# Kernel optimization log

Hardware: AMD Instinct MI355X
Metric: run time of the kernel (lower is better)

## Reference

```python
import jax, jax.numpy as jnp
import numpy as np
from jax import lax

N, XD, L, D, R = 32768, 8, 16, 64, 64
HID_E, HID_N, MIX = 256, 512, 32
LOG2PI = float(np.log(2.0 * np.pi))


def setup_inputs() -> dict:
    key = jax.random.key(0)
    ks = jax.random.split(key, 18)
    g = lambda k, shape, s: (jax.random.normal(k, shape, jnp.float32) * s)
    init_std = 0.001
    return {
        "X": jax.random.normal(ks[0], (N, XD, L), jnp.float32),
        "init_w": g(ks[1], (1, R), init_std),
        "cores": g(ks[2], (L, R, D, R), init_std),          # core_list stacked
        "enc1_w": g(ks[3], (HID_E, XD), 1.0 / np.sqrt(XD)),
        "enc1_b": jnp.zeros((HID_E,), jnp.float32),
        "enc2_w": g(ks[4], (D, HID_E), 1.0 / np.sqrt(HID_E)),
        "enc2_b": jnp.zeros((D,), jnp.float32),
        "nade_w1": g(ks[5], (HID_N, R), 1.0 / np.sqrt(R)),
        "nade_b1": jnp.zeros((HID_N,), jnp.float32),
        "nade_w2": g(ks[6], (R, HID_N), 1.0 / np.sqrt(HID_N)),
        "nade_b2": jnp.zeros((R,), jnp.float32),
        "mu_w": g(ks[7], (MIX * XD, R), 1.0 / np.sqrt(R)),
        "mu_b": jnp.zeros((MIX * XD,), jnp.float32),
        "sig_w": g(ks[8], (MIX * XD, R), 1.0 / np.sqrt(R)),
        "sig_b": jnp.zeros((MIX * XD,), jnp.float32),
        "alpha_w": g(ks[9], (MIX, R), 1.0 / np.sqrt(R)),
        "alpha_b": jnp.zeros((MIX,), jnp.float32),
    }


def _encode(x, enc1_w, enc1_b, enc2_w, enc2_b):
    # x: [..., xd] -> [..., d]  (NADE-style input encoder)
    h = jax.nn.relu(x @ enc1_w.T + enc1_b)
    return h @ enc2_w.T + enc2_b


def _phi(x, h, nade_w1, nade_b1, nade_w2, nade_b2,
         mu_w, mu_b, sig_w, sig_b, alpha_w, alpha_b):
    # x: [n, xd], h: [n, r] hidden state -> [n] mixture-of-Gaussians log-density
    n = x.shape[0]
    h = jax.nn.relu(h @ nade_w1.T + nade_b1)
    h = jax.nn.relu(h @ nade_w2.T + nade_b2)
    mu = (h @ mu_w.T + mu_b).reshape(n, MIX, XD)
    log_sig = (h @ sig_w.T + sig_b).reshape(n, MIX, XD)
    sig = jnp.exp(log_sig)
    log_alpha = jax.nn.log_softmax(h @ alpha_w.T + alpha_b, axis=-1)  # [n, MIX]
    z = (x[:, None, :] - mu) / sig
    comp_lp = jnp.sum(-0.5 * z * z - log_sig - 0.5 * LOG2PI, axis=-1)  # [n, MIX]
    return jax.nn.logsumexp(log_alpha + comp_lp, axis=-1)


def reference(X, init_w, cores, enc1_w, enc1_b, enc2_w, enc2_b,
              nade_w1, nade_b1, nade_w2, nade_b2,
              mu_w, mu_b, sig_w, sig_b, alpha_w, alpha_b):
    n = X.shape[0]
    xseq = jnp.transpose(X, (2, 0, 1))                      # [L, n, xd]
    enc_all = _encode(xseq, enc1_w, enc1_b, enc2_w, enc2_b)  # [L, n, d]
    phi = lambda x, h: _phi(x, h, nade_w1, nade_b1, nade_w2, nade_b2,
                            mu_w, mu_b, sig_w, sig_b, alpha_w, alpha_b)

    tmp0 = jnp.broadcast_to(init_w, (n, R))
    res0 = phi(xseq[0], tmp0)
    norm0 = jnp.sum(tmp0 * tmp0)

    def step(tmp, inp):
        enc_prev, core_prev, x_cur = inp
        tmp = jnp.einsum('nd,ni,idj->nj', enc_prev, tmp, core_prev)
        return tmp, (phi(x_cur, tmp), jnp.sum(tmp * tmp))

    xs = (enc_all[:L - 1], cores[:L - 1], xseq[1:])
    _, (res_steps, norm_steps) = lax.scan(step, tmp0, xs)
    result = res0 + jnp.sum(res_steps, axis=0)   # [n] log-likelihood
    norm = norm0 + jnp.sum(norm_steps)           # scalar Frobenius norm accumulator
    return result, norm
```

## Files before the change

### kernel.cpp

```cpp
#include <hip/hip_runtime.h>

typedef unsigned short u16;
typedef unsigned int u32;
typedef __attribute__((ext_vector_type(8))) __bf16 bf16x8;
typedef __attribute__((ext_vector_type(4))) float f32x4;

#define NSAMP 32768
#define HALF_LOG2PI 0.91893853320467274f

#define O_W1N 0
#define O_W2N 32768
#define O_MUW 65536
#define O_SGW 81920
#define O_ALW 98304
#define O_E1W 100352
#define O_E2W 108544
#define O_CORT 124928
#define CORT_STEP 262144
#define WS_U16 4057088

#define LH1A 0
#define LH1B 8192
#define LCLP 0
#define LALP 8192
#define LH2  16384
#define LXP  24576
#define LENC 32768
#define LTMPA 49152
#define LTMPB 57344
#define LXT  65536
#define XTS 66
#define LDS_BYTES 67648

static __device__ __forceinline__ u16 f2b(float x){ return __builtin_bit_cast(u16,(__bf16)x); }
static __device__ __forceinline__ float b2f(u16 u){ return __builtin_bit_cast(float,((u32)u)<<16); }
static __device__ __forceinline__ u32 pk2(float lo, float hi){
  return (u32)__builtin_bit_cast(u16,(__bf16)lo) | ((u32)__builtin_bit_cast(u16,(__bf16)hi)<<16);
}
static __device__ __forceinline__ f32x4 MF(uint4 a, uint4 b, f32x4 c){
  union U{uint4 q; bf16x8 v;};
  U A, B; A.q=a; B.q=b;
  return __builtin_amdgcn_mfma_f32_16x16x32_bf16(A.v, B.v, c, 0, 0, 0);
}

__global__ void prep_w(const float* __restrict__ nw1, const float* __restrict__ nw2,
                       const float* __restrict__ muw, const float* __restrict__ sgw,
                       const float* __restrict__ alw, const float* __restrict__ e1w,
                       const float* __restrict__ e2w, u16* __restrict__ ws,
                       float* __restrict__ out) {
  int idx0 = blockIdx.x * blockDim.x + threadIdx.x;
  int stride = gridDim.x * blockDim.x;
  for (int idx = idx0; idx < 124928; idx += stride) {
    float v;
    if      (idx < 32768)  v = nw1[idx];
    else if (idx < 65536)  v = nw2[idx - 32768];
    else if (idx < 81920)  v = muw[idx - 65536];
    else if (idx < 98304)  v = sgw[idx - 81920];
    else if (idx < 100352) v = alw[idx - 98304];
    else if (idx < 108544) { int j = idx - 100352; int o = j >> 5, k = j & 31;
                             v = (k < 8) ? e1w[o*8 + k] : 0.0f; }
    else                   v = e2w[idx - 108544];
    ws[idx] = f2b(v);
  }
  if (idx0 == 0) out[NSAMP] = 0.0f;
}

__global__ void prep_core(const float* __restrict__ cores, u16* __restrict__ ws) {
  int t = blockIdx.x >> 6, i = blockIdx.x & 63;
  __shared__ float T[64][65];
  const float* src = cores + ((size_t)(t*64 + i)*64)*64;
  for (int idx = threadIdx.x; idx < 4096; idx += 256) {
    int d = idx >> 6, j = idx & 63;
    T[d][j] = src[d*64 + j];
  }
  __syncthreads();
  u16* dst = ws + O_CORT + (size_t)t*CORT_STEP + (size_t)i*64;
  for (int idx = threadIdx.x; idx < 4096; idx += 256) {
    int j = idx >> 6, d = idx & 63;
    dst[(size_t)j*4096 + d] = f2b(T[d][j]);
  }
}

__global__ __launch_bounds__(256, 2)
void fused(const float* __restrict__ X, const float* __restrict__ init_w,
           const float* __restrict__ b1e, const float* __restrict__ b2e,
           const float* __restrict__ b1n, const float* __restrict__ b2n,
           const float* __restrict__ mub, const float* __restrict__ sgb,
           const float* __restrict__ alb, const u16* __restrict__ ws,
           float* __restrict__ out) {
  __shared__ __align__(16) char Lp[LDS_BYTES];
  const int tid = threadIdx.x;
  const int w = tid >> 6, l = tid & 63, li = l & 15, g = l >> 4;
  const int n0 = blockIdx.x * 64;
  const int sw = (li & 7) << 4;
  float res = 0.f, nrm = 0.f;

  char* TMPc = Lp + LTMPA;
  char* TMPn = Lp + LTMPB;

  for (int idx = tid; idx < 4096; idx += 256) {
    int s = idx >> 6, r = idx & 63;
    *(u16*)(TMPc + s*128 + ((2*r) ^ ((s & 7) << 4))) = f2b(init_w[r]);
  }
  { uint4 z = {0,0,0,0};
    for (int idx = tid; idx < 512; idx += 256) *(uint4*)(Lp + LXP + idx*16) = z; }
  if (tid < 64) { float v = init_w[tid]; nrm += 64.f * v * v; }
  __syncthreads();

  for (int t = 0; t < 16; ++t) {
    for (int idx = tid; idx < 512; idx += 256) {
      int s = idx & 63, d = idx >> 6;
      float x = X[(size_t)(n0 + s)*128 + d*16 + t];
      *(float*)(Lp + LXT + (d*XTS + s)*4) = x;
      *(u16*)(Lp + LXP + s*128 + ((2*d) ^ ((s & 7) << 4))) = f2b(x);
    }
    __syncthreads();

    f32x4 acc2[4];
#pragma unroll
    for (int st = 0; st < 4; ++st) acc2[st] = (f32x4){0.f,0.f,0.f,0.f};
#pragma unroll 1
    for (int oc = 0; oc < 8; ++oc) {
      const u16* a0 = ws + O_W1N + (oc*64 + w*16 + li)*64 + 8*g;
      uint4 af0 = *(const uint4*)a0;
      uint4 af1 = *(const uint4*)(a0 + 32);
      char* H1b = Lp + ((oc & 1) ? LH1B : LH1A);
      float4 bb = *(const float4*)(b1n + oc*64 + w*16 + 4*g);
#pragma unroll
      for (int st = 0; st < 4; ++st) {
        int s = st*16 + li;
        uint4 b0 = *(const uint4*)(TMPc + s*128 + ((16*g) ^ sw));
        uint4 b1 = *(const uint4*)(TMPc + s*128 + ((64 + 16*g) ^ sw));
        f32x4 a1 = (f32x4){0.f,0.f,0.f,0.f};
        a1 = MF(af0, b0, a1); a1 = MF(af1, b1, a1);
        float v0 = fmaxf(a1[0] + bb.x, 0.f), v1 = fmaxf(a1[1] + bb.y, 0.f);
        float v2 = fmaxf(a1[2] + bb.z, 0.f), v3 = fmaxf(a1[3] + bb.w, 0.f);
        *(u32*)(H1b + s*128 + ((32*w + 8*g) ^ sw))     = pk2(v0, v1);
        *(u32*)(H1b + s*128 + ((32*w + 8*g + 4) ^ sw)) = pk2(v2, v3);
      }
      __syncthreads();
      const u16* a2 = ws + O_W2N + (w*16 + li)*512 + oc*64 + 8*g;
      uint4 c0 = *(const uint4*)a2;
      uint4 c1 = *(const uint4*)(a2 + 32);
#pragma unroll
      for (int st = 0; st < 4; ++st) {
        int s = st*16 + li;
        uint4 b0 = *(const uint4*)(H1b + s*128 + ((16*g) ^ sw));
        uint4 b1 = *(const uint4*)(H1b + s*128 + ((64 + 16*g) ^ sw));
        acc2[st] = MF(c0, b0, acc2[st]); acc2[st] = MF(c1, b1, acc2[st]);
      }
    }
    {
      float4 bb = *(const float4*)(b2n + w*16 + 4*g);
#pragma unroll
      for (int st = 0; st < 4; ++st) {
        int s = st*16 + li;
        float v0 = fmaxf(acc2[st][0] + bb.x, 0.f), v1 = fmaxf(acc2[st][1] + bb.y, 0.f);
        float v2 = fmaxf(acc2[st][2] + bb.z, 0.f), v3 = fmaxf(acc2[st][3] + bb.w, 0.f);
        *(u32*)(Lp + LH2 + s*128 + ((32*w + 8*g) ^ sw))     = pk2(v0, v1);
        *(u32*)(Lp + LH2 + s*128 + ((32*w + 8*g + 4) ^ sw)) = pk2(v2, v3);
      }
    }
    __syncthreads();

#pragma unroll 1
    for (int c = 0; c < 4; ++c) {
      int ob = c*64 + w*16;
      const u16* as_ = ws + O_SGW + (ob + li)*64 + 8*g;
      const u16* am_ = ws + O_MUW + (ob + li)*64 + 8*g;
      uint4 sf0 = *(const uint4*)as_, sf1 = *(const uint4*)(as_ + 32);
      uint4 mf0 = *(const uint4*)am_, mf1 = *(const uint4*)(am_ + 32);
      float4 bs = *(const float4*)(sgb + ob + 4*g);
      float4 bm = *(const float4*)(mub + ob + 4*g);
      const float bsv[4] = {bs.x, bs.y, bs.z, bs.w};
      const float bmv[4] = {bm.x, bm.y, bm.z, bm.w};
#pragma unroll
      for (int st = 0; st < 4; ++st) {
        int s = st*16 + li;
        uint4 b0 = *(const uint4*)(Lp + LH2 + s*128 + ((16*g) ^ sw));
        uint4 b1 = *(const uint4*)(Lp + LH2 + s*128 + ((64 + 16*g) ^ sw));
        f32x4 aS = (f32x4){0.f,0.f,0.f,0.f}, aM = (f32x4){0.f,0.f,0.f,0.f};
        aS = MF(sf0, b0, aS); aS = MF(sf1, b1, aS);
        aM = MF(mf0, b0, aM); aM = MF(mf1, b1, aM);
        float part = 0.f;
#pragma unroll
        for (int r = 0; r < 4; ++r) {
          int d = (4*g + r) & 7;
          float ls = aS[r] + bsv[r];
          float mu = aM[r] + bmv[r];
          float xv = *(const float*)(Lp + LXT + (d*XTS + s)*4);
          float z = (xv - mu) * __expf(-ls);
          part += -0.5f*z*z - ls - HALF_LOG2PI;
        }
        float comb = part + __shfl_xor(part, 16);
        if (!(g & 1)) {
          int mix = c*8 + 2*w + (g >> 1);
          *(float*)(Lp + LCLP + (mix*64 + s)*4) = comb;
        }
      }
    }
    {
      int s = w*16 + li;
#pragma unroll
      for (int ot = 0; ot < 2; ++ot) {
        const u16* aa = ws + O_ALW + (ot*16 + li)*64 + 8*g;
        uint4 a0 = *(const uint4*)aa, a1 = *(const uint4*)(aa + 32);
        uint4 b0 = *(const uint4*)(Lp + LH2 + s*128 + ((16*g) ^ sw));
        uint4 b1 = *(const uint4*)(Lp + LH2 + s*128 + ((64 + 16*g) ^ sw));
        f32x4 acc = (f32x4){0.f,0.f,0.f,0.f};
        acc = MF(a0, b0, acc); acc = MF(a1, b1, acc);
        float4 ab4 = *(const float4*)(alb + ot*16 + 4*g);
        const float abv[4] = {ab4.x, ab4.y, ab4.z, ab4.w};
#pragma unroll
        for (int r = 0; r < 4; ++r)
          *(float*)(Lp + LALP + ((ot*16 + 4*g + r)*64 + s)*4) = acc[r] + abv[r];
      }
    }
    __syncthreads();

    if (tid < 64) {
      float m1 = -1e30f, m2 = -1e30f;
#pragma unroll 1
      for (int m = 0; m < 32; ++m) {
        float a  = *(const float*)(Lp + LALP + (m*64 + tid)*4);
        float cc = *(const float*)(Lp + LCLP + (m*64 + tid)*4);
        m1 = fmaxf(m1, a + cc); m2 = fmaxf(m2, a);
      }
      float s1 = 0.f, s2 = 0.f;
#pragma unroll 1
      for (int m = 0; m < 32; ++m) {
        float a  = *(const float*)(Lp + LALP + (m*64 + tid)*4);
        float cc = *(const float*)(Lp + LCLP + (m*64 + tid)*4);
        s1 += __expf(a + cc - m1); s2 += __expf(a - m2);
      }
      res += (m1 + __logf(s1)) - (m2 + __logf(s2));
    }
    if (t == 15) break;
    __syncthreads();

    f32x4 acE[4];
#pragma unroll
    for (int st = 0; st < 4; ++st) acE[st] = (f32x4){0.f,0.f,0.f,0.f};
#pragma unroll 1
    for (int ec = 0; ec < 4; ++ec) {
      const u16* ae_ = ws + O_E1W + (ec*64 + w*16 + li)*32 + 8*g;
      uint4 ae = *(const uint4*)ae_;
      char* H1b = Lp + ((ec & 1) ? LH1B : LH1A);
      float4 bb = *(const float4*)(b1e + ec*64 + w*16 + 4*g);
#pragma unroll
      for (int st = 0; st < 4; ++st) {
        int s = st*16 + li;
        uint4 b0 = *(const uint4*)(Lp + LXP + s*128 + ((16*g) ^ sw));
        f32x4 ah = (f32x4){0.f,0.f,0.f,0.f};
        ah = MF(ae, b0, ah);
        float v0 = fmaxf(ah[0] + bb.x, 0.f), v1 = fmaxf(ah[1] + bb.y, 0.f);
        float v2 = fmaxf(ah[2] + bb.z, 0.f), v3 = fmaxf(ah[3] + bb.w, 0.f);
        *(u32*)(H1b + s*128 + ((32*w + 8*g) ^ sw))     = pk2(v0, v1);
        *(u32*)(H1b + s*128 + ((32*w + 8*g + 4) ^ sw)) = pk2(v2, v3);
      }
      __syncthreads();
      const u16* a2 = ws + O_E2W + (w*16 + li)*256 + ec*64 + 8*g;
      uint4 c0 = *(const uint4*)a2, c1 = *(const uint4*)(a2 + 32);
#pragma unroll
      for (int st = 0; st < 4; ++st) {
        int s = st*16 + li;
        uint4 b0 = *(const uint4*)(H1b + s*128 + ((16*g) ^ sw));
        uint4 b1 = *(const uint4*)(H1b + s*128 + ((64 + 16*g) ^ sw));
        acE[st] = MF(c0, b0, acE[st]); acE[st] = MF(c1, b1, acE[st]);
      }
    }
    {
      float4 be = *(const float4*)(b2e + w*16 + 4*g);
      const float bev[4] = {be.x, be.y, be.z, be.w};
#pragma unroll
      for (int st = 0; st < 4; ++st) {
        int s = st*16 + li;
#pragma unroll
        for (int r = 0; r < 4; ++r)
          *(float*)(Lp + LENC + s*256 + ((64*w + 16*g + 4*r) ^ sw)) = acE[st][r] + bev[r];
      }
    }
    __syncthreads();

    f32x4 aU[4];
#pragma unroll
    for (int st = 0; st < 4; ++st) aU[st] = (f32x4){0.f,0.f,0.f,0.f};
    const u16* cort = ws + O_CORT + (size_t)t*CORT_STEP + (w*16 + li)*4096;
    const int bs_ = tid >> 2, bq = tid & 3;
    const int bsw = (bs_ & 7) << 4;
    auto BUILD = [&](int c) {
      int i  = 2*c + (bq >> 1);
      int d0 = (bq & 1) * 32;
      float ts = b2f(*(const u16*)(TMPc + bs_*128 + ((2*i) ^ bsw)));
      char* dst = Lp + ((c & 1) ? 16384 : 0) + bs_*256;
      const char* ef = Lp + LENC + bs_*256;
#pragma unroll
      for (int jj = 0; jj < 4; ++jj) {
        float4 e0 = *(const float4*)(ef + ((4*(d0 + 8*jj))     ^ bsw));
        float4 e1 = *(const float4*)(ef + ((4*(d0 + 8*jj + 4)) ^ bsw));
        uint4 o;
        o.x = pk2(ts*e0.x, ts*e0.y);
        o.y = pk2(ts*e0.z, ts*e0.w);
        o.z = pk2(ts*e1.x, ts*e1.y);
        o.w = pk2(ts*e1.z, ts*e1.w);
        *(uint4*)(dst + ((64*bq + 16*jj) ^ bsw)) = o;
      }
    };
    BUILD(0);
    __syncthreads();
    uint4 a0 = *(const uint4*)(cort + 8*g);
    uint4 a1 = *(const uint4*)(cort + 32 + 8*g);
    uint4 a2 = *(const uint4*)(cort + 64 + 8*g);
    uint4 a3 = *(const uint4*)(cort + 96 + 8*g);
#pragma unroll 1
    for (int c = 0; c < 32; ++c) {
      uint4 na0 = a0, na1 = a1, na2 = a2, na3 = a3;
      if (c < 31) {
        const u16* cn = cort + (c + 1)*128;
        na0 = *(const uint4*)(cn + 8*g);
        na1 = *(const uint4*)(cn + 32 + 8*g);
        na2 = *(const uint4*)(cn + 64 + 8*g);
        na3 = *(const uint4*)(cn + 96 + 8*g);
        BUILD(c + 1);
      }
      const char* Bb = Lp + ((c & 1) ? 16384 : 0);
#pragma unroll
      for (int st = 0; st < 4; ++st) {
        int s = st*16 + li;
        const char* bp = Bb + s*256;
        aU[st] = MF(a0, *(const uint4*)(bp + ((16*g) ^ sw)), aU[st]);
        aU[st] = MF(a1, *(const uint4*)(bp + ((64  + 16*g) ^ sw)), aU[st]);
        aU[st] = MF(a2, *(const uint4*)(bp + ((128 + 16*g) ^ sw)), aU[st]);
        aU[st] = MF(a3, *(const uint4*)(bp + ((192 + 16*g) ^ sw)), aU[st]);
      }
      __syncthreads();
      a0 = na0; a1 = na1; a2 = na2; a3 = na3;
    }
#pragma unroll
    for (int st = 0; st < 4; ++st) {
      int s = st*16 + li;
      nrm += aU[st][0]*aU[st][0] + aU[st][1]*aU[st][1]
           + aU[st][2]*aU[st][2] + aU[st][3]*aU[st][3];
      *(u32*)(TMPn + s*128 + ((32*w + 8*g) ^ sw))     = pk2(aU[st][0], aU[st][1]);
      *(u32*)(TMPn + s*128 + ((32*w + 8*g + 4) ^ sw)) = pk2(aU[st][2], aU[st][3]);
    }
    { uint4 z = {0,0,0,0};
      for (int idx = tid; idx < 512; idx += 256) *(uint4*)(Lp + LXP + idx*16) = z; }
    __syncthreads();
    { char* tt = TMPc; TMPc = TMPn; TMPn = tt; }
  }

  if (tid < 64) out[n0 + tid] = res;
  __syncthreads();
  *(float*)(Lp + LCLP + tid*4) = nrm;
  __syncthreads();
  if (tid < 64) {
    float v = *(const float*)(Lp + LCLP + tid*4)
            + *(const float*)(Lp + LCLP + (tid + 64)*4)
            + *(const float*)(Lp + LCLP + (tid + 128)*4)
            + *(const float*)(Lp + LCLP + (tid + 192)*4);
#pragma unroll
    for (int off = 32; off > 0; off >>= 1) v += __shfl_down(v, off);
    if (tid == 0) atomicAdd(out + NSAMP, v);
  }
}

extern "C" void kernel_launch(void* const* d_in, const int* in_sizes, int n_in,
                              void* d_out, int out_size, void* d_ws, size_t ws_size,
                              hipStream_t stream) {
  const float* X      = (const float*)d_in[0];
  const float* init_w = (const float*)d_in[1];
  const float* cores  = (const float*)d_in[2];
  const float* e1w    = (const float*)d_in[3];
  const float* b1e    = (const float*)d_in[4];
  const float* e2w    = (const float*)d_in[5];
  const float* b2e    = (const float*)d_in[6];
  const float* nw1    = (const float*)d_in[7];
  const float* b1n    = (const float*)d_in[8];
  const float* nw2    = (const float*)d_in[9];
  const float* b2n    = (const float*)d_in[10];
  const float* muw    = (const float*)d_in[11];
  const float* mub    = (const float*)d_in[12];
  const float* sgw    = (const float*)d_in[13];
  const float* sgb    = (const float*)d_in[14];
  const float* alw    = (const float*)d_in[15];
  const float* alb    = (const float*)d_in[16];
  float* out = (float*)d_out;
  u16*   ws  = (u16*)d_ws;

  prep_w<<<64, 256, 0, stream>>>(nw1, nw2, muw, sgw, alw, e1w, e2w, ws, out);
  prep_core<<<960, 256, 0, stream>>>(cores, ws);
  fused<<<NSAMP/64, 256, 0, stream>>>(X, init_w, b1e, b2e, b1n, b2n,
                                      mub, sgb, alb, ws, out);
}
```

Before: 971.5 us.

## Split-K core contraction across waves, software-pipeline MLP stages, parallelize logsumexp

The TT core contraction now splits the K dimension (i*64+d) across the four waves, with each wave computing all 64 outputs. B fragments are built in registers instead of being staged through double-buffered LDS with a barrier per chunk. Partial sums are reduced through LDS in bf16, and the core weights are pre-permuted into an MFMA-fragment layout. The two-layer NADE and encoder MLPs are software-pipelined so layer 1 of chunk p overlaps layer 2 of chunk p-1 with a single barrier per step, and the mixture logsumexp is spread over all four waves instead of one. The main intent is to remove per-chunk barriers and the serial single-wave reduction. In exchange it uses more LDS (80KB), more accumulator registers, and bf16 rounding of the partial sums.

```diff
diff --git a/kernel.cpp b/kernel.cpp
--- a/kernel.cpp
+++ b/kernel.cpp
@@ -17,23 +17,30 @@
 #define O_E2W 108544
 #define O_CORT 124928
 #define CORT_STEP 262144
-#define WS_U16 4057088
-
-#define LH1A 0
-#define LH1B 8192
-#define LCLP 0
-#define LALP 8192
-#define LH2  16384
-#define LXP  24576
-#define LENC 32768
-#define LTMPA 49152
-#define LTMPB 57344
-#define LXT  65536
-#define XTS 66
-#define LDS_BYTES 67648
+
+#define L_H1A 0
+#define L_H1B 8192
+#define L_LM1 0
+#define L_LM2 1024
+#define L_LS1 8192
+#define L_LS2 9216
+#define L_PRA 0
+#define L_PRB 8192
+#define L_PRC 16384
+#define L_H2  16384
+#define L_CLP 24576
+#define L_ALP 32768
+#define L_XT  40960
+#define L_XP  43008
+#define L_TMPA 49152
+#define L_TMPB 57344
+#define L_ENC 65536
+#define LDS_BYTES 81920
 
 static __device__ __forceinline__ u16 f2b(float x){ return __builtin_bit_cast(u16,(__bf16)x); }
 static __device__ __forceinline__ float b2f(u16 u){ return __builtin_bit_cast(float,((u32)u)<<16); }
+static __device__ __forceinline__ float b2flo(u32 v){ return __builtin_bit_cast(float, v<<16); }
+static __device__ __forceinline__ float b2fhi(u32 v){ return __builtin_bit_cast(float, v & 0xffff0000u); }
 static __device__ __forceinline__ u32 pk2(float lo, float hi){
   return (u32)__builtin_bit_cast(u16,(__bf16)lo) | ((u32)__builtin_bit_cast(u16,(__bf16)hi)<<16);
 }
@@ -67,17 +74,15 @@
 
 __global__ void prep_core(const float* __restrict__ cores, u16* __restrict__ ws) {
   int t = blockIdx.x >> 6, i = blockIdx.x & 63;
-  __shared__ float T[64][65];
-  const float* src = cores + ((size_t)(t*64 + i)*64)*64;
+  const float* src = cores + ((size_t)(t*64 + i) * 64) * 64;
+  u16* dst = ws + O_CORT + (size_t)t * CORT_STEP;
   for (int idx = threadIdx.x; idx < 4096; idx += 256) {
     int d = idx >> 6, j = idx & 63;
-    T[d][j] = src[d*64 + j];
-  }
-  __syncthreads();
-  u16* dst = ws + O_CORT + (size_t)t*CORT_STEP + (size_t)i*64;
-  for (int idx = threadIdx.x; idx < 4096; idx += 256) {
-    int j = idx >> 6, d = idx & 63;
-    dst[(size_t)j*4096 + d] = f2b(T[d][j]);
+    float v = src[d*64 + j];
+    int k = i*64 + d;
+    int kk = k >> 5, g = (k >> 3) & 3, b = k & 7;
+    int ot = j >> 4, li = j & 15;
+    dst[(size_t)(((kk*4 + ot)*64) + g*16 + li)*8 + b] = f2b(v);
   }
 }
 
@@ -91,64 +96,70 @@
   __shared__ __align__(16) char Lp[LDS_BYTES];
   const int tid = threadIdx.x;
   const int w = tid >> 6, l = tid & 63, li = l & 15, g = l >> 4;
+  const int e3 = li & 7;
+  const int sw = e3 << 4;
   const int n0 = blockIdx.x * 64;
-  const int sw = (li & 7) << 4;
   float res = 0.f, nrm = 0.f;
 
-  char* TMPc = Lp + LTMPA;
-  char* TMPn = Lp + LTMPB;
+  char* TMPc = Lp + L_TMPA;
+  char* TMPn = Lp + L_TMPB;
 
   for (int idx = tid; idx < 4096; idx += 256) {
     int s = idx >> 6, r = idx & 63;
     *(u16*)(TMPc + s*128 + ((2*r) ^ ((s & 7) << 4))) = f2b(init_w[r]);
   }
   { uint4 z = {0,0,0,0};
-    for (int idx = tid; idx < 512; idx += 256) *(uint4*)(Lp + LXP + idx*16) = z; }
+    *(uint4*)(Lp + L_XP + tid*16) = z; }
   if (tid < 64) { float v = init_w[tid]; nrm += 64.f * v * v; }
   __syncthreads();
 
   for (int t = 0; t < 16; ++t) {
     for (int idx = tid; idx < 512; idx += 256) {
-      int s = idx & 63, d = idx >> 6;
+      int d = idx >> 6, s = idx & 63;
       float x = X[(size_t)(n0 + s)*128 + d*16 + t];
-      *(float*)(Lp + LXT + (d*XTS + s)*4) = x;
-      *(u16*)(Lp + LXP + s*128 + ((2*d) ^ ((s & 7) << 4))) = f2b(x);
-    }
-    __syncthreads();
+      *(float*)(Lp + L_XT + (d*64 + s)*4) = x;
+      *(u16*)(Lp + L_XP + s*64 + ((2*d) ^ ((s & 3) << 4))) = f2b(x);
+    }
 
     f32x4 acc2[4];
 #pragma unroll
     for (int st = 0; st < 4; ++st) acc2[st] = (f32x4){0.f,0.f,0.f,0.f};
 #pragma unroll 1
-    for (int oc = 0; oc < 8; ++oc) {
-      const u16* a0 = ws + O_W1N + (oc*64 + w*16 + li)*64 + 8*g;
-      uint4 af0 = *(const uint4*)a0;
-      uint4 af1 = *(const uint4*)(a0 + 32);
-      char* H1b = Lp + ((oc & 1) ? LH1B : LH1A);
-      float4 bb = *(const float4*)(b1n + oc*64 + w*16 + 4*g);
-#pragma unroll
-      for (int st = 0; st < 4; ++st) {
-        int s = st*16 + li;
-        uint4 b0 = *(const uint4*)(TMPc + s*128 + ((16*g) ^ sw));
-        uint4 b1 = *(const uint4*)(TMPc + s*128 + ((64 + 16*g) ^ sw));
-        f32x4 a1 = (f32x4){0.f,0.f,0.f,0.f};
-        a1 = MF(af0, b0, a1); a1 = MF(af1, b1, a1);
-        float v0 = fmaxf(a1[0] + bb.x, 0.f), v1 = fmaxf(a1[1] + bb.y, 0.f);
-        float v2 = fmaxf(a1[2] + bb.z, 0.f), v3 = fmaxf(a1[3] + bb.w, 0.f);
-        *(u32*)(H1b + s*128 + ((32*w + 8*g) ^ sw))     = pk2(v0, v1);
-        *(u32*)(H1b + s*128 + ((32*w + 8*g + 4) ^ sw)) = pk2(v2, v3);
+    for (int p = 0; p <= 8; ++p) {
+      if (p < 8) {
+        const u16* a0p = ws + O_W1N + (p*64 + w*16 + li)*64 + 8*g;
+        uint4 af0 = *(const uint4*)a0p;
+        uint4 af1 = *(const uint4*)(a0p + 32);
+        float4 bb = *(const float4*)(b1n + p*64 + w*16 + 4*g);
+        char* H1b = Lp + ((p & 1) ? L_H1B : L_H1A);
+#pragma unroll
+        for (int st = 0; st < 4; ++st) {
+          int s = st*16 + li;
+          uint4 b0 = *(const uint4*)(TMPc + s*128 + ((16*g) ^ sw));
+          uint4 b1 = *(const uint4*)(TMPc + s*128 + ((64 + 16*g) ^ sw));
+          f32x4 a1 = (f32x4){0.f,0.f,0.f,0.f};
+          a1 = MF(af0, b0, a1); a1 = MF(af1, b1, a1);
+          float v0 = fmaxf(a1[0] + bb.x, 0.f), v1 = fmaxf(a1[1] + bb.y, 0.f);
+          float v2 = fmaxf(a1[2] + bb.z, 0.f), v3 = fmaxf(a1[3] + bb.w, 0.f);
+          *(u32*)(H1b + s*128 + ((32*w + 8*g) ^ sw))     = pk2(v0, v1);
+          *(u32*)(H1b + s*128 + ((32*w + 8*g + 4) ^ sw)) = pk2(v2, v3);
+        }
+      }
+      if (p > 0) {
+        int q = p - 1;
+        const u16* a2p = ws + O_W2N + (w*16 + li)*512 + q*64 + 8*g;
+        uint4 c0 = *(const uint4*)a2p;
+        uint4 c1 = *(const uint4*)(a2p + 32);
+        const char* H1r = Lp + ((q & 1) ? L_H1B : L_H1A);
+#pragma unroll
+        for (int st = 0; st < 4; ++st) {
+          int s = st*16 + li;
+          uint4 b0 = *(const uint4*)(H1r + s*128 + ((16*g) ^ sw));
+          uint4 b1 = *(const uint4*)(H1r + s*128 + ((64 + 16*g) ^ sw));
+          acc2[st] = MF(c0, b0, acc2[st]); acc2[st] = MF(c1, b1, acc2[st]);
+        }
       }
       __syncthreads();
-      const u16* a2 = ws + O_W2N + (w*16 + li)*512 + oc*64 + 8*g;
-      uint4 c0 = *(const uint4*)a2;
-      uint4 c1 = *(const uint4*)(a2 + 32);
-#pragma unroll
-      for (int st = 0; st < 4; ++st) {
-        int s = st*16 + li;
-        uint4 b0 = *(const uint4*)(H1b + s*128 + ((16*g) ^ sw));
-        uint4 b1 = *(const uint4*)(H1b + s*128 + ((64 + 16*g) ^ sw));
-        acc2[st] = MF(c0, b0, acc2[st]); acc2[st] = MF(c1, b1, acc2[st]);
-      }
     }
     {
       float4 bb = *(const float4*)(b2n + w*16 + 4*g);
@@ -157,8 +168,8 @@
         int s = st*16 + li;
         float v0 = fmaxf(acc2[st][0] + bb.x, 0.f), v1 = fmaxf(acc2[st][1] + bb.y, 0.f);
         float v2 = fmaxf(acc2[st][2] + bb.z, 0.f), v3 = fmaxf(acc2[st][3] + bb.w, 0.f);
-        *(u32*)(Lp + LH2 + s*128 + ((32*w + 8*g) ^ sw))     = pk2(v0, v1);
-        *(u32*)(Lp + LH2 + s*128 + ((32*w + 8*g + 4) ^ sw)) = pk2(v2, v3);
+        *(u32*)(Lp + L_H2 + s*128 + ((32*w + 8*g) ^ sw))     = pk2(v0, v1);
+        *(u32*)(Lp + L_H2 + s*128 + ((32*w + 8*g + 4) ^ sw)) = pk2(v2, v3);
       }
     }
     __syncthreads();
@@ -172,13 +183,13 @@
       uint4 mf0 = *(const uint4*)am_, mf1 = *(const uint4*)(am_ + 32);
       float4 bs = *(const float4*)(sgb + ob + 4*g);
       float4 bm = *(const float4*)(mub + ob + 4*g);
-      const float bsv[4] = {bs.x, bs.y, bs.z, bs.w};
-      const float bmv[4] = {bm.x, bm.y, bm.z, bm.w};
+      const float bsv[4] = {bs.x,bs.y,bs.z,bs.w};
+      const float bmv[4] = {bm.x,bm.y,bm.z,bm.w};
 #pragma unroll
       for (int st = 0; st < 4; ++st) {
         int s = st*16 + li;
-        uint4 b0 = *(const uint4*)(Lp + LH2 + s*128 + ((16*g) ^ sw));
-        uint4 b1 = *(const uint4*)(Lp + LH2 + s*128 + ((64 + 16*g) ^ sw));
+        uint4 b0 = *(const uint4*)(Lp + L_H2 + s*128 + ((16*g) ^ sw));
+        uint4 b1 = *(const uint4*)(Lp + L_H2 + s*128 + ((64 + 16*g) ^ sw));
         f32x4 aS = (f32x4){0.f,0.f,0.f,0.f}, aM = (f32x4){0.f,0.f,0.f,0.f};
         aS = MF(sf0, b0, aS); aS = MF(sf1, b1, aS);
         aM = MF(mf0, b0, aM); aM = MF(mf1, b1, aM);
@@ -188,14 +199,14 @@
           int d = (4*g + r) & 7;
           float ls = aS[r] + bsv[r];
           float mu = aM[r] + bmv[r];
-          float xv = *(const float*)(Lp + LXT + (d*XTS + s)*4);
+          float xv = *(const float*)(Lp + L_XT + (d*64 + s)*4);
           float z = (xv - mu) * __expf(-ls);
           part += -0.5f*z*z - ls - HALF_LOG2PI;
         }
         float comb = part + __shfl_xor(part, 16);
         if (!(g & 1)) {
           int mix = c*8 + 2*w + (g >> 1);
-          *(float*)(Lp + LCLP + (mix*64 + s)*4) = comb;
+          *(float*)(Lp + L_CLP + (mix*64 + s)*4) = comb;
         }
       }
     }
@@ -205,160 +216,238 @@
       for (int ot = 0; ot < 2; ++ot) {
         const u16* aa = ws + O_ALW + (ot*16 + li)*64 + 8*g;
         uint4 a0 = *(const uint4*)aa, a1 = *(const uint4*)(aa + 32);
-        uint4 b0 = *(const uint4*)(Lp + LH2 + s*128 + ((16*g) ^ sw));
-        uint4 b1 = *(const uint4*)(Lp + LH2 + s*128 + ((64 + 16*g) ^ sw));
+        uint4 b0 = *(const uint4*)(Lp + L_H2 + s*128 + ((16*g) ^ sw));
+        uint4 b1 = *(const uint4*)(Lp + L_H2 + s*128 + ((64 + 16*g) ^ sw));
         f32x4 acc = (f32x4){0.f,0.f,0.f,0.f};
         acc = MF(a0, b0, acc); acc = MF(a1, b1, acc);
         float4 ab4 = *(const float4*)(alb + ot*16 + 4*g);
         const float abv[4] = {ab4.x, ab4.y, ab4.z, ab4.w};
 #pragma unroll
         for (int r = 0; r < 4; ++r)
-          *(float*)(Lp + LALP + ((ot*16 + 4*g + r)*64 + s)*4) = acc[r] + abv[r];
+          *(float*)(Lp + L_ALP + ((ot*16 + 4*g + r)*64 + s)*4) = acc[r] + abv[r];
       }
     }
     __syncthreads();
 
+    float g1, g2;
+    {
+      int s = l;
+      float m1 = -1e30f, m2 = -1e30f;
+#pragma unroll
+      for (int mm = 0; mm < 8; ++mm) {
+        int m = w*8 + mm;
+        float a = *(const float*)(Lp + L_ALP + (m*64 + s)*4);
+        float c = *(const float*)(Lp + L_CLP + (m*64 + s)*4);
+        m1 = fmaxf(m1, a + c); m2 = fmaxf(m2, a);
+      }
+      *(float*)(Lp + L_LM1 + (w*64 + s)*4) = m1;
+      *(float*)(Lp + L_LM2 + (w*64 + s)*4) = m2;
+      __syncthreads();
+      g1 = fmaxf(fmaxf(*(const float*)(Lp + L_LM1 + s*4),
+                       *(const float*)(Lp + L_LM1 + (64 + s)*4)),
+                 fmaxf(*(const float*)(Lp + L_LM1 + (128 + s)*4),
+                       *(const float*)(Lp + L_LM1 + (192 + s)*4)));
+      g2 = fmaxf(fmaxf(*(const float*)(Lp + L_LM2 + s*4),
+                       *(const float*)(Lp + L_LM2 + (64 + s)*4)),
+                 fmaxf(*(const float*)(Lp + L_LM2 + (128 + s)*4),
+                       *(const float*)(Lp + L_LM2 + (192 + s)*4)));
+      float s1 = 0.f, s2 = 0.f;
+#pragma unroll
+      for (int mm = 0; mm < 8; ++mm) {
+        int m = w*8 + mm;
+        float a = *(const float*)(Lp + L_ALP + (m*64 + s)*4);
+        float c = *(const float*)(Lp + L_CLP + (m*64 + s)*4);
+        s1 += __expf(a + c - g1); s2 += __expf(a - g2);
+      }
+      *(float*)(Lp + L_LS1 + (w*64 + s)*4) = s1;
+      *(float*)(Lp + L_LS2 + (w*64 + s)*4) = s2;
+      __syncthreads();
+    }
     if (tid < 64) {
-      float m1 = -1e30f, m2 = -1e30f;
-#pragma unroll 1
-      for (int m = 0; m < 32; ++m) {
-        float a  = *(const float*)(Lp + LALP + (m*64 + tid)*4);
-        float cc = *(const float*)(Lp + LCLP + (m*64 + tid)*4);
-        m1 = fmaxf(m1, a + cc); m2 = fmaxf(m2, a);
-      }
-      float s1 = 0.f, s2 = 0.f;
-#pragma unroll 1
-      for (int m = 0; m < 32; ++m) {
-        float a  = *(const float*)(Lp + LALP + (m*64 + tid)*4);
-        float cc = *(const float*)(Lp + LCLP + (m*64 + tid)*4);
-        s1 += __expf(a + cc - m1); s2 += __expf(a - m2);
-      }
-      res += (m1 + __logf(s1)) - (m2 + __logf(s2));
+      float s1 = *(const float*)(Lp + L_LS1 + tid*4)
+               + *(const float*)(Lp + L_LS1 + (64 + tid)*4)
+               + *(const float*)(Lp + L_LS1 + (128 + tid)*4)
+               + *(const float*)(Lp + L_LS1 + (192 + tid)*4);
+      float s2 = *(const float*)(Lp + L_LS2 + tid*4)
+               + *(const float*)(Lp + L_LS2 + (64 + tid)*4)
+               + *(const float*)(Lp + L_LS2 + (128 + tid)*4)
+               + *(const float*)(Lp + L_LS2 + (192 + tid)*4);
+      res += (g1 + __logf(s1)) - (g2 + __logf(s2));
     }
     if (t == 15) break;
-    __syncthreads();
 
     f32x4 acE[4];
 #pragma unroll
     for (int st = 0; st < 4; ++st) acE[st] = (f32x4){0.f,0.f,0.f,0.f};
 #pragma unroll 1
-    for (int ec = 0; ec < 4; ++ec) {
-      const u16* ae_ = ws + O_E1W + (ec*64 + w*16 + li)*32 + 8*g;
-      uint4 ae = *(const uint4*)ae_;
-      char* H1b = Lp + ((ec & 1) ? LH1B : LH1A);
-      float4 bb = *(const float4*)(b1e + ec*64 + w*16 + 4*g);
+    for (int p = 0; p <= 4; ++p) {
+      if (p < 4) {
+        const u16* aep = ws + O_E1W + (p*64 + w*16 + li)*32 + 8*g;
+        uint4 ae = *(const uint4*)aep;
+        float4 bb = *(const float4*)(b1e + p*64 + w*16 + 4*g);
+        char* H1b = Lp + ((p & 1) ? L_H1B : L_H1A);
+#pragma unroll
+        for (int st = 0; st < 4; ++st) {
+          int s = st*16 + li;
+          uint4 b0 = *(const uint4*)(Lp + L_XP + s*64 + ((16*g) ^ ((s & 3) << 4)));
+          f32x4 ah = (f32x4){0.f,0.f,0.f,0.f};
+          ah = MF(ae, b0, ah);
+          float v0 = fmaxf(ah[0] + bb.x, 0.f), v1 = fmaxf(ah[1] + bb.y, 0.f);
+          float v2 = fmaxf(ah[2] + bb.z, 0.f), v3 = fmaxf(ah[3] + bb.w, 0.f);
+          *(u32*)(H1b + s*128 + ((32*w + 8*g) ^ sw))     = pk2(v0, v1);
+          *(u32*)(H1b + s*128 + ((32*w + 8*g + 4) ^ sw)) = pk2(v2, v3);
+        }
+      }
+      if (p > 0) {
+        int q = p - 1;
+        const u16* c0p = ws + O_E2W + (w*16 + li)*256 + q*64 + 8*g;
+        uint4 c0 = *(const uint4*)c0p, c1 = *(const uint4*)(c0p + 32);
+        const char* H1r = Lp + ((q & 1) ? L_H1B : L_H1A);
+#pragma unroll
+        for (int st = 0; st < 4; ++st) {
+          int s = st*16 + li;
+          uint4 b0 = *(const uint4*)(H1r + s*128 + ((16*g) ^ sw));
+          uint4 b1 = *(const uint4*)(H1r + s*128 + ((64 + 16*g) ^ sw));
+          acE[st] = MF(c0, b0, acE[st]); acE[st] = MF(c1, b1, acE[st]);
+        }
+      }
+      if (p == 4) {
+        float4 be = *(const float4*)(b2e + w*16 + 4*g);
+        const float bev[4] = {be.x, be.y, be.z, be.w};
+#pragma unroll
+        for (int st = 0; st < 4; ++st) {
+          int s = st*16 + li;
+#pragma unroll
+          for (int r = 0; r < 4; ++r) {
+            int d = w*16 + 4*g + r;
+            *(float*)(Lp + L_ENC + s*256 + ((((d >> 3) ^ e3)) << 5) + ((d & 7) << 2))
+                = acE[st][r] + bev[r];
+          }
+        }
+      }
+      __syncthreads();
+    }
+
+    f32x4 aU[4][4];
+#pragma unroll
+    for (int ot = 0; ot < 4; ++ot)
+#pragma unroll
+      for (int st = 0; st < 4; ++st) aU[ot][st] = (f32x4){0.f,0.f,0.f,0.f};
+
+    const u16* Abase = ws + O_CORT + (size_t)t*CORT_STEP + (size_t)(w*32)*2048 + (size_t)l*8;
+    uint4 A0 = *(const uint4*)(Abase);
+    uint4 A1 = *(const uint4*)(Abase + 512);
+    uint4 A2 = *(const uint4*)(Abase + 1024);
+    uint4 A3 = *(const uint4*)(Abase + 1536);
+#pragma unroll 1
+    for (int kk = 0; kk < 32; ++kk) {
+      uint4 nA0, nA1, nA2, nA3;
+      if (kk < 31) {
+        const u16* ap = Abase + (size_t)(kk + 1)*2048;
+        nA0 = *(const uint4*)(ap);
+        nA1 = *(const uint4*)(ap + 512);
+        nA2 = *(const uint4*)(ap + 1024);
+        nA3 = *(const uint4*)(ap + 1536);
+      }
+      int kwa = w*32 + kk;
+      int h = kwa & 1;
+      int tof = (kwa & ~1) ^ sw;
+      int eof = ((((h << 2) | g) ^ e3) << 5);
+      uint4 B[4];
 #pragma unroll
       for (int st = 0; st < 4; ++st) {
         int s = st*16 + li;
-        uint4 b0 = *(const uint4*)(Lp + LXP + s*128 + ((16*g) ^ sw));
-        f32x4 ah = (f32x4){0.f,0.f,0.f,0.f};
-        ah = MF(ae, b0, ah);
-        float v0 = fmaxf(ah[0] + bb.x, 0.f), v1 = fmaxf(ah[1] + bb.y, 0.f);
-        float v2 = fmaxf(ah[2] + bb.z, 0.f), v3 = fmaxf(ah[3] + bb.w, 0.f);
-        *(u32*)(H1b + s*128 + ((32*w + 8*g) ^ sw))     = pk2(v0, v1);
-        *(u32*)(H1b + s*128 + ((32*w + 8*g + 4) ^ sw)) = pk2(v2, v3);
-      }
-      __syncthreads();
-      const u16* a2 = ws + O_E2W + (w*16 + li)*256 + ec*64 + 8*g;
-      uint4 c0 = *(const uint4*)a2, c1 = *(const uint4*)(a2 + 32);
-#pragma unroll
-      for (int st = 0; st < 4; ++st) {
+        float ts = b2f(*(const u16*)(TMPc + s*128 + tof));
+        const char* ep = Lp + L_ENC + s*256 + eof;
+        float4 e0 = *(const float4*)(ep);
+        float4 e1 = *(const float4*)(ep + 16);
+        uint4 bb;
+        bb.x = pk2(ts*e0.x, ts*e0.y); bb.y = pk2(ts*e0.z, ts*e0.w);
+        bb.z = pk2(ts*e1.x, ts*e1.y); bb.w = pk2(ts*e1.z, ts*e1.w);
+        B[st] = bb;
+      }
+      __builtin_amdgcn_s_setprio(1);
+#pragma unroll
+      for (int ot = 0; ot < 4; ++ot) {
+        uint4 Af = (ot == 0) ? A0 : (ot == 1) ? A1 : (ot == 2) ? A2 : A3;
+#pragma unroll
+        for (int st = 0; st < 4; ++st)
+          aU[ot][st] = MF(Af, B[st], aU[ot][st]);
+      }
+      __builtin_amdgcn_s_setprio(0);
+      A0 = nA0; A1 = nA1; A2 = nA2; A3 = nA3;
+    }
+
+    if (w >= 2) {
+      char* pr = Lp + ((w == 2) ? L_PRA : L_PRB);
+#pragma unroll
+      for (int ot = 0; ot < 4; ++ot)
+#pragma unroll
+        for (int st = 0; st < 4; ++st) {
+          uint2 pv;
+          pv.x = pk2(aU[ot][st][0], aU[ot][st][1]);
+          pv.y = pk2(aU[ot][st][2], aU[ot][st][3]);
+          *(uint2*)(pr + (st*16 + li)*128 + 8*(((ot << 2) | g) ^ e3)) = pv;
+        }
+    }
+    __syncthreads();
+    if (w < 2) {
+      const char* pr = Lp + ((w == 0) ? L_PRA : L_PRB);
+#pragma unroll
+      for (int ot = 0; ot < 4; ++ot)
+#pragma unroll
+        for (int st = 0; st < 4; ++st) {
+          uint2 pv = *(const uint2*)(pr + (st*16 + li)*128 + 8*(((ot << 2) | g) ^ e3));
+          aU[ot][st][0] += b2flo(pv.x); aU[ot][st][1] += b2fhi(pv.x);
+          aU[ot][st][2] += b2flo(pv.y); aU[ot][st][3] += b2fhi(pv.y);
+        }
+      int stb = (w == 0) ? 2 : 0;
+#pragma unroll
+      for (int sto = 0; sto < 2; ++sto) {
+        int st = stb + sto;
+#pragma unroll
+        for (int ot = 0; ot < 4; ++ot) {
+          uint2 pv;
+          pv.x = pk2(aU[ot][st][0], aU[ot][st][1]);
+          pv.y = pk2(aU[ot][st][2], aU[ot][st][3]);
+          *(uint2*)(Lp + L_PRC + (st*16 + li)*128 + 8*(((ot << 2) | g) ^ e3)) = pv;
+        }
+      }
+    }
+    __syncthreads();
+    if (w < 2) {
+      int stb = (w == 0) ? 0 : 2;
+#pragma unroll
+      for (int sto = 0; sto < 2; ++sto) {
+        int st = stb + sto;
         int s = st*16 + li;
-        uint4 b0 = *(const uint4*)(H1b + s*128 + ((16*g) ^ sw));
-        uint4 b1 = *(const uint4*)(H1b + s*128 + ((64 + 16*g) ^ sw));
-        acE[st] = MF(c0, b0, acE[st]); acE[st] = MF(c1, b1, acE[st]);
-      }
-    }
-    {
-      float4 be = *(const float4*)(b2e + w*16 + 4*g);
-      const float bev[4] = {be.x, be.y, be.z, be.w};
-#pragma unroll
-      for (int st = 0; st < 4; ++st) {
-        int s = st*16 + li;
-#pragma unroll
-        for (int r = 0; r < 4; ++r)
-          *(float*)(Lp + LENC + s*256 + ((64*w + 16*g + 4*r) ^ sw)) = acE[st][r] + bev[r];
-      }
-    }
-    __syncthreads();
-
-    f32x4 aU[4];
-#pragma unroll
-    for (int st = 0; st < 4; ++st) aU[st] = (f32x4){0.f,0.f,0.f,0.f};
-    const u16* cort = ws + O_CORT + (size_t)t*CORT_STEP + (w*16 + li)*4096;
-    const int bs_ = tid >> 2, bq = tid & 3;
-    const int bsw = (bs_ & 7) << 4;
-    auto BUILD = [&](int c) {
-      int i  = 2*c + (bq >> 1);
-      int d0 = (bq & 1) * 32;
-      float ts = b2f(*(const u16*)(TMPc + bs_*128 + ((2*i) ^ bsw)));
-      char* dst = Lp + ((c & 1) ? 16384 : 0) + bs_*256;
-      const char* ef = Lp + LENC + bs_*256;
-#pragma unroll
-      for (int jj = 0; jj < 4; ++jj) {
-        float4 e0 = *(const float4*)(ef + ((4*(d0 + 8*jj))     ^ bsw));
-        float4 e1 = *(const float4*)(ef + ((4*(d0 + 8*jj + 4)) ^ bsw));
-        uint4 o;
-        o.x = pk2(ts*e0.x, ts*e0.y);
-        o.y = pk2(ts*e0.z, ts*e0.w);
-        o.z = pk2(ts*e1.x, ts*e1.y);
-        o.w = pk2(ts*e1.z, ts*e1.w);
-        *(uint4*)(dst + ((64*bq + 16*jj) ^ bsw)) = o;
-      }
-    };
-    BUILD(0);
-    __syncthreads();
-    uint4 a0 = *(const uint4*)(cort + 8*g);
-    uint4 a1 = *(const uint4*)(cort + 32 + 8*g);
-    uint4 a2 = *(const uint4*)(cort + 64 + 8*g);
-    uint4 a3 = *(const uint4*)(cort + 96 + 8*g);
-#pragma unroll 1
-    for (int c = 0; c < 32; ++c) {
-      uint4 na0 = a0, na1 = a1, na2 = a2, na3 = a3;
-      if (c < 31) {
-        const u16* cn = cort + (c + 1)*128;
-        na0 = *(const uint4*)(cn + 8*g);
-        na1 = *(const uint4*)(cn + 32 + 8*g);
-        na2 = *(const uint4*)(cn + 64 + 8*g);
-        na3 = *(const uint4*)(cn + 96 + 8*g);
-        BUILD(c + 1);
-      }
-      const char* Bb = Lp + ((c & 1) ? 16384 : 0);
-#pragma unroll
-      for (int st = 0; st < 4; ++st) {
-        int s = st*16 + li;
-        const char* bp = Bb + s*256;
-        aU[st] = MF(a0, *(const uint4*)(bp + ((16*g) ^ sw)), aU[st]);
-        aU[st] = MF(a1, *(const uint4*)(bp + ((64  + 16*g) ^ sw)), aU[st]);
-        aU[st] = MF(a2, *(const uint4*)(bp + ((128 + 16*g) ^ sw)), aU[st]);
-        aU[st] = MF(a3, *(const uint4*)(bp + ((192 + 16*g) ^ sw)), aU[st]);
-      }
-      __syncthreads();
-      a0 = na0; a1 = na1; a2 = na2; a3 = na3;
-    }
-#pragma unroll
-    for (int st = 0; st < 4; ++st) {
-      int s = st*16 + li;
-      nrm += aU[st][0]*aU[st][0] + aU[st][1]*aU[st][1]
-           + aU[st][2]*aU[st][2] + aU[st][3]*aU[st][3];
-      *(u32*)(TMPn + s*128 + ((32*w + 8*g) ^ sw))     = pk2(aU[st][0], aU[st][1]);
-      *(u32*)(TMPn + s*128 + ((32*w + 8*g + 4) ^ sw)) = pk2(aU[st][2], aU[st][3]);
-    }
-    { uint4 z = {0,0,0,0};
-      for (int idx = tid; idx < 512; idx += 256) *(uint4*)(Lp + LXP + idx*16) = z; }
+#pragma unroll
+        for (int ot = 0; ot < 4; ++ot) {
+          uint2 pv = *(const uint2*)(Lp + L_PRC + (st*16 + li)*128 + 8*(((ot << 2) | g) ^ e3));
+          float v0 = aU[ot][st][0] + b2flo(pv.x);
+          float v1 = aU[ot][st][1] + b2fhi(pv.x);
+          float v2 = aU[ot][st][2] + b2flo(pv.y);
+          float v3 = aU[ot][st][3] + b2fhi(pv.y);
+          nrm += v0*v0 + v1*v1 + v2*v2 + v3*v3;
+          *(u32*)(TMPn + s*128 + ((32*ot + 8*g) ^ sw))     = pk2(v0, v1);
+          *(u32*)(TMPn + s*128 + ((32*ot + 8*g + 4) ^ sw)) = pk2(v2, v3);
+        }
+      }
+    }
     __syncthreads();
     { char* tt = TMPc; TMPc = TMPn; TMPn = tt; }
   }
 
   if (tid < 64) out[n0 + tid] = res;
+
   __syncthreads();
-  *(float*)(Lp + LCLP + tid*4) = nrm;
+  *(float*)(Lp + tid*4) = nrm;
   __syncthreads();
   if (tid < 64) {
-    float v = *(const float*)(Lp + LCLP + tid*4)
-            + *(const float*)(Lp + LCLP + (tid + 64)*4)
-            + *(const float*)(Lp + LCLP + (tid + 128)*4)
-            + *(const float*)(Lp + LCLP + (tid + 192)*4);
+    float v = *(const float*)(Lp + tid*4)
+            + *(const float*)(Lp + (tid + 64)*4)
+            + *(const float*)(Lp + (tid + 128)*4)
+            + *(const float*)(Lp + (tid + 192)*4);
 #pragma unroll
     for (int off = 32; off > 0; off >>= 1) v += __shfl_down(v, off);
     if (tid == 0) atomicAdd(out + NSAMP, v);
```

Measured after the change: 928.3 us. 4.4% less time.
